# Kernel optimization log

Measured on AMD Instinct MI355X. Metric: run time of the kernel, lower is better.

Reference implementation:

```python
import jax, jax.numpy as jnp
import numpy as np

# Lorenz parameters (fixed in LorenzSDE.__init__)
SIGMA = 10.0
RHO = 28.0
BETA = 8.0 / 3.0
NOISE = 2.0      # σ diffusion scale (diffusion = σ * I_3, additive)
T = 0.05
DT = 0.01
N_STEPS = 5      # T / DT, ConstantStepSize (no stepsize_controller passed)
BATCH = 4194304


def _drift(y):
    # y: [..., 3] Lorenz vector field
    x_, y_, z_ = y[..., 0], y[..., 1], y[..., 2]
    return jnp.stack(
        [SIGMA * (y_ - x_), x_ * (RHO - z_) - y_, x_ * y_ - BETA * z_], axis=-1
    )


def setup_inputs() -> dict:
    key = jax.random.key(0)
    k1, k2, k3 = jax.random.split(key, 3)
    x = jax.random.normal(k1, (BATCH, 3), dtype=jnp.float32)
    # standard normals; scaled inside reference to Brownian increment / Levy area
    dW = jax.random.normal(k2, (BATCH, N_STEPS, 3), dtype=jnp.float32)
    dH = jax.random.normal(k3, (BATCH, N_STEPS, 3), dtype=jnp.float32)
    return {"x": x, "dW": dW, "dH": dH}


def reference(x, dW, dH):
    # ShARK (Shifted Additive-noise Runge-Kutta), strong order 1.5 for additive
    # noise, two drift evaluations per step (diffrax.ShARK with constant steps):
    #   z1 = y + g*H
    #   z2 = y + (5/6)*h*f(z1) + g*((5/6)*W + H)
    #   y1 = y + h*(0.4*f(z1) + 0.6*f(z2)) + g*W
    # where W ~ N(0, h I), H (space-time Levy area) ~ N(0, h/12 I), g = NOISE*I.
    dt = jnp.float32(DT)
    gW = jnp.moveaxis(dW, 1, 0) * (NOISE * jnp.sqrt(dt))          # [n, B, 3]
    gH = jnp.moveaxis(dH, 1, 0) * (NOISE * jnp.sqrt(dt / 12.0))   # [n, B, 3]

    def step(y, wh):
        w, h = wh
        z1 = y + h
        f1 = _drift(z1)
        z2 = y + (5.0 / 6.0) * dt * f1 + (5.0 / 6.0) * w + h
        f2 = _drift(z2)
        y1 = y + dt * (0.4 * f1 + 0.6 * f2) + w
        return y1, None

    yT, _ = jax.lax.scan(step, x, (gW, gH))
    return yT  # [B, 3] final state (sol.ys saves t1 only)
```

## Files before the change

kernel.cpp:

```cpp
#include <hip/hip_runtime.h>


#define NSTEPS 5
#define BLOCK 256
#define WPB 4
#define TILE 64

__global__ __launch_bounds__(BLOCK) void lorenz_shark(
    const float* __restrict__ x,
    const float* __restrict__ dW,
    const float* __restrict__ dH,
    float* __restrict__ out)
{
    __shared__ float s_w[WPB][TILE * 15];
    __shared__ float s_h[WPB][TILE * 15];
    __shared__ float s_x[WPB][TILE * 3];

    const int lane = threadIdx.x & 63;
    const int wv   = threadIdx.x >> 6;
    const long long ptBase = ((long long)blockIdx.x * WPB + wv) * TILE;

    const float4* gw = (const float4*)(dW + ptBase * 15);
    const float4* gh = (const float4*)(dH + ptBase * 15);
    const float4* gx = (const float4*)(x  + ptBase * 3);

    float4* lw = (float4*)s_w[wv];
    float4* lh = (float4*)s_h[wv];
    float4* lx = (float4*)s_x[wv];

#pragma unroll
    for (int k = 0; k < 3; ++k) {
        lw[lane + k * 64] = gw[lane + k * 64];
        lh[lane + k * 64] = gh[lane + k * 64];
    }
    if (lane < 48) {
        lw[lane + 192] = gw[lane + 192];
        lh[lane + 192] = gh[lane + 192];
        lx[lane]       = gx[lane];
    }
    __builtin_amdgcn_wave_barrier();

    float a = s_x[wv][3 * lane + 0];
    float b = s_x[wv][3 * lane + 1];
    float c = s_x[wv][3 * lane + 2];

    const float cW    = 0.2f;
    const float cH    = 0.05773502691896258f;
    const float dt    = 0.01f;
    const float c56   = 5.0f / 6.0f;
    const float c56dt = c56 * dt;
    const float SIGMA = 10.0f;
    const float RHO   = 28.0f;
    const float BETA  = 8.0f / 3.0f;

#pragma unroll
    for (int n = 0; n < NSTEPS; ++n) {
        const int w0 = 15 * lane + 3 * n;
        const float wa = s_w[wv][w0 + 0] * cW;
        const float wb = s_w[wv][w0 + 1] * cW;
        const float wc = s_w[wv][w0 + 2] * cW;
        const float ha = s_h[wv][w0 + 0] * cH;
        const float hb = s_h[wv][w0 + 1] * cH;
        const float hc = s_h[wv][w0 + 2] * cH;

        const float z1a = a + ha, z1b = b + hb, z1c = c + hc;
        const float f1a = SIGMA * (z1b - z1a);
        const float f1b = z1a * (RHO - z1c) - z1b;
        const float f1c = z1a * z1b - BETA * z1c;

        const float z2a = a + c56dt * f1a + c56 * wa + ha;
        const float z2b = b + c56dt * f1b + c56 * wb + hb;
        const float z2c = c + c56dt * f1c + c56 * wc + hc;
        const float f2a = SIGMA * (z2b - z2a);
        const float f2b = z2a * (RHO - z2c) - z2b;
        const float f2c = z2a * z2b - BETA * z2c;

        a = a + dt * (0.4f * f1a + 0.6f * f2a) + wa;
        b = b + dt * (0.4f * f1b + 0.6f * f2b) + wb;
        c = c + dt * (0.4f * f1c + 0.6f * f2c) + wc;
    }

    s_x[wv][3 * lane + 0] = a;
    s_x[wv][3 * lane + 1] = b;
    s_x[wv][3 * lane + 2] = c;
    __builtin_amdgcn_wave_barrier();

    float4* go = (float4*)(out + ptBase * 3);
    if (lane < 48) go[lane] = lx[lane];
}

extern "C" void kernel_launch(void* const* d_in, const int* in_sizes, int n_in,
                              void* d_out, int out_size, void* d_ws, size_t ws_size,
                              hipStream_t stream) {
    const float* x  = (const float*)d_in[0];
    const float* dW = (const float*)d_in[1];
    const float* dH = (const float*)d_in[2];
    float* out = (float*)d_out;

    const int batch   = in_sizes[0] / 3;
    const int nblocks = batch / (WPB * TILE);

    hipLaunchKernelGGL(lorenz_shark, dim3(nblocks), dim3(BLOCK), 0, stream,
                       x, dW, dH, out);
}
```

Before: 518.7 us.

## Replace LDS-staged coalesced loads with per-thread direct loads in grid-stride loop

Drops the shared-memory staging of the dW/dH/x tiles. Each thread now reads its own 15-float rows straight from global memory using four overlapping 4-byte-aligned float4-sized structs and writes its 3 outputs directly. The launch becomes a grid-stride loop capped at 2048 blocks with an occupancy hint. This removes LDS traffic and wave barriers, but the global accesses are strided and uncoalesced (60-byte stride per lane), which the cache has to absorb.

```diff
diff --git a/kernel.cpp b/kernel.cpp
--- a/kernel.cpp
+++ b/kernel.cpp
@@ -1,48 +1,22 @@
 #include <hip/hip_runtime.h>
+#include <stdint.h>
 
 
-#define NSTEPS 5
 #define BLOCK 256
-#define WPB 4
-#define TILE 64
+#define MAXBLOCKS 2048
 
-__global__ __launch_bounds__(BLOCK) void lorenz_shark(
+struct __attribute__((aligned(4))) F4 { float x, y, z, w; };
+struct __attribute__((aligned(4))) F2 { float x, y; };
+struct __attribute__((aligned(4))) F3 { float x, y, z; };
+
+__global__ __launch_bounds__(BLOCK, 8) void lorenz_shark(
     const float* __restrict__ x,
     const float* __restrict__ dW,
     const float* __restrict__ dH,
-    float* __restrict__ out)
+    float* __restrict__ out,
+    int batch)
 {
-    __shared__ float s_w[WPB][TILE * 15];
-    __shared__ float s_h[WPB][TILE * 15];
-    __shared__ float s_x[WPB][TILE * 3];
-
-    const int lane = threadIdx.x & 63;
-    const int wv   = threadIdx.x >> 6;
-    const long long ptBase = ((long long)blockIdx.x * WPB + wv) * TILE;
-
-    const float4* gw = (const float4*)(dW + ptBase * 15);
-    const float4* gh = (const float4*)(dH + ptBase * 15);
-    const float4* gx = (const float4*)(x  + ptBase * 3);
-
-    float4* lw = (float4*)s_w[wv];
-    float4* lh = (float4*)s_h[wv];
-    float4* lx = (float4*)s_x[wv];
-
-#pragma unroll
-    for (int k = 0; k < 3; ++k) {
-        lw[lane + k * 64] = gw[lane + k * 64];
-        lh[lane + k * 64] = gh[lane + k * 64];
-    }
-    if (lane < 48) {
-        lw[lane + 192] = gw[lane + 192];
-        lh[lane + 192] = gh[lane + 192];
-        lx[lane]       = gx[lane];
-    }
-    __builtin_amdgcn_wave_barrier();
-
-    float a = s_x[wv][3 * lane + 0];
-    float b = s_x[wv][3 * lane + 1];
-    float c = s_x[wv][3 * lane + 2];
+    const int nthreads = gridDim.x * BLOCK;
 
     const float cW    = 0.2f;
     const float cH    = 0.05773502691896258f;
@@ -53,40 +27,50 @@
     const float RHO   = 28.0f;
     const float BETA  = 8.0f / 3.0f;
 
-#pragma unroll
-    for (int n = 0; n < NSTEPS; ++n) {
-        const int w0 = 15 * lane + 3 * n;
-        const float wa = s_w[wv][w0 + 0] * cW;
-        const float wb = s_w[wv][w0 + 1] * cW;
-        const float wc = s_w[wv][w0 + 2] * cW;
-        const float ha = s_h[wv][w0 + 0] * cH;
-        const float hb = s_h[wv][w0 + 1] * cH;
-        const float hc = s_h[wv][w0 + 2] * cH;
+#define STEP(WA,WB,WC,HA,HB,HC) do {                                  \
+        const float wa=(WA)*cW, wb=(WB)*cW, wc=(WC)*cW;               \
+        const float ha=(HA)*cH, hb=(HB)*cH, hc=(HC)*cH;               \
+        const float z1a=a+ha, z1b=b+hb, z1c=c+hc;                     \
+        const float f1a=SIGMA*(z1b-z1a);                              \
+        const float f1b=z1a*(RHO-z1c)-z1b;                            \
+        const float f1c=z1a*z1b-BETA*z1c;                             \
+        const float z2a=a+c56dt*f1a+c56*wa+ha;                        \
+        const float z2b=b+c56dt*f1b+c56*wb+hb;                        \
+        const float z2c=c+c56dt*f1c+c56*wc+hc;                        \
+        const float f2a=SIGMA*(z2b-z2a);                              \
+        const float f2b=z2a*(RHO-z2c)-z2b;                            \
+        const float f2c=z2a*z2b-BETA*z2c;                             \
+        a=a+dt*(0.4f*f1a+0.6f*f2a)+wa;                                \
+        b=b+dt*(0.4f*f1b+0.6f*f2b)+wb;                                \
+        c=c+dt*(0.4f*f1c+0.6f*f2c)+wc;                                \
+    } while (0)
 
-        const float z1a = a + ha, z1b = b + hb, z1c = c + hc;
-        const float f1a = SIGMA * (z1b - z1a);
-        const float f1b = z1a * (RHO - z1c) - z1b;
-        const float f1c = z1a * z1b - BETA * z1c;
+    for (int pt = blockIdx.x * BLOCK + threadIdx.x; pt < batch; pt += nthreads) {
+        const float* wp = dW + (size_t)pt * 15;
+        const float* hp = dH + (size_t)pt * 15;
+        const float* xp = x  + (size_t)pt * 3;
 
-        const float z2a = a + c56dt * f1a + c56 * wa + ha;
-        const float z2b = b + c56dt * f1b + c56 * wb + hb;
-        const float z2c = c + c56dt * f1c + c56 * wc + hc;
-        const float f2a = SIGMA * (z2b - z2a);
-        const float f2b = z2a * (RHO - z2c) - z2b;
-        const float f2c = z2a * z2b - BETA * z2c;
+        const F4 w0 = *(const F4*)(wp);
+        const F4 w1 = *(const F4*)(wp + 4);
+        const F4 w2 = *(const F4*)(wp + 8);
+        const F4 w3 = *(const F4*)(wp + 11);
+        const F4 h0 = *(const F4*)(hp);
+        const F4 h1 = *(const F4*)(hp + 4);
+        const F4 h2 = *(const F4*)(hp + 8);
+        const F4 h3 = *(const F4*)(hp + 11);
+        const F2 xab = *(const F2*)(xp);
+        float a = xab.x, b = xab.y, c = xp[2];
 
-        a = a + dt * (0.4f * f1a + 0.6f * f2a) + wa;
-        b = b + dt * (0.4f * f1b + 0.6f * f2b) + wb;
-        c = c + dt * (0.4f * f1c + 0.6f * f2c) + wc;
+        STEP(w0.x, w0.y, w0.z,  h0.x, h0.y, h0.z);
+        STEP(w0.w, w1.x, w1.y,  h0.w, h1.x, h1.y);
+        STEP(w1.z, w1.w, w2.x,  h1.z, h1.w, h2.x);
+        STEP(w2.y, w2.z, w2.w,  h2.y, h2.z, h2.w);
+        STEP(w3.y, w3.z, w3.w,  h3.y, h3.z, h3.w);
+
+        F3 r; r.x = a; r.y = b; r.z = c;
+        *(F3*)(out + (size_t)pt * 3) = r;
     }
-
-    s_x[wv][3 * lane + 0] = a;
-    s_x[wv][3 * lane + 1] = b;
-    s_x[wv][3 * lane + 2] = c;
-    __builtin_amdgcn_wave_barrier();
-
-    float4* go = (float4*)(out + ptBase * 3);
-    if (lane < 48) go[lane] = lx[lane];
+#undef STEP
 }
 
 extern "C" void kernel_launch(void* const* d_in, const int* in_sizes, int n_in,
@@ -97,9 +81,10 @@
     const float* dH = (const float*)d_in[2];
     float* out = (float*)d_out;
 
-    const int batch   = in_sizes[0] / 3;
-    const int nblocks = batch / (WPB * TILE);
+    const int batch = in_sizes[0] / 3;
+    int nblocks = (batch + BLOCK - 1) / BLOCK;
+    if (nblocks > MAXBLOCKS) nblocks = MAXBLOCKS;
 
     hipLaunchKernelGGL(lorenz_shark, dim3(nblocks), dim3(BLOCK), 0, stream,
-                       x, dW, dH, out);
+                       x, dW, dH, out, batch);
 }
```

Result: no change. 526.7 us (+1.5%).
